# Performance work log

Hardware: AMD Instinct MI355X
Metric: run time of the kernel (lower is better)

The kernel has to match this reference:

```python
import jax, jax.numpy as jnp
import numpy as np

B, S, D = 2, 2048, 2048
H, KV, HD = 16, 8, 128
EPS = 1e-6
NEG = -1e9


def rms_norm(x, w, eps=EPS):
    # per-head RMSNorm over last dim, computed in fp32 like the torch module
    xf = x.astype(jnp.float32)
    var = jnp.mean(xf * xf, axis=-1, keepdims=True)
    return (w * (xf * jax.lax.rsqrt(var + eps)).astype(x.dtype))


def rotate_half(x):
    x1, x2 = jnp.split(x, 2, axis=-1)
    return jnp.concatenate((-x2, x1), axis=-1)


def setup_inputs() -> dict:
    key = jax.random.key(0)
    ks = jax.random.split(key, 8)
    hidden_states = jax.random.normal(ks[0], (B, S, D), dtype=jnp.float32)
    # RoPE tables (rope_theta=10000), shape [B, S, HD]
    inv_freq = 1.0 / (10000.0 ** (np.arange(0, HD, 2, dtype=np.float32) / HD))
    t = np.arange(S, dtype=np.float32)
    freqs = np.outer(t, inv_freq)                      # [S, HD/2]
    emb = np.concatenate([freqs, freqs], axis=-1)      # [S, HD]
    cos = jnp.broadcast_to(jnp.cos(emb)[None], (B, S, HD)).astype(jnp.float32)
    sin = jnp.broadcast_to(jnp.sin(emb)[None], (B, S, HD)).astype(jnp.float32)
    # additive causal mask [B, 1, S, S]
    causal = jnp.triu(jnp.full((S, S), NEG, dtype=jnp.float32), k=1)
    attention_mask = jnp.broadcast_to(causal[None, None], (B, 1, S, S))
    scale = 0.02
    Wq = jax.random.normal(ks[1], (D, H * HD), dtype=jnp.float32) * scale
    Wk = jax.random.normal(ks[2], (D, KV * HD), dtype=jnp.float32) * scale
    Wv = jax.random.normal(ks[3], (D, KV * HD), dtype=jnp.float32) * scale
    Wo = jax.random.normal(ks[4], (H * HD, D), dtype=jnp.float32) * scale
    q_norm_w = jnp.ones((HD,), dtype=jnp.float32)
    k_norm_w = jnp.ones((HD,), dtype=jnp.float32)
    return {"hidden_states": hidden_states, "cos": cos, "sin": sin,
            "attention_mask": attention_mask, "Wq": Wq, "Wk": Wk, "Wv": Wv,
            "Wo": Wo, "q_norm_w": q_norm_w, "k_norm_w": k_norm_w}


def reference(hidden_states, cos, sin, attention_mask, Wq, Wk, Wv, Wo, q_norm_w, k_norm_w):
    b, s, _ = hidden_states.shape
    scaling = HD ** -0.5
    n_rep = H // KV
    q = (hidden_states @ Wq).reshape(b, s, H, HD)
    k = (hidden_states @ Wk).reshape(b, s, KV, HD)
    v = (hidden_states @ Wv).reshape(b, s, KV, HD)
    # per-head RMSNorm then [B, heads, S, HD]
    q = rms_norm(q, q_norm_w).transpose(0, 2, 1, 3)
    k = rms_norm(k, k_norm_w).transpose(0, 2, 1, 3)
    v = v.transpose(0, 2, 1, 3)
    # RoPE (cos/sin unsqueezed on head axis)
    c = cos[:, None, :, :]
    sn = sin[:, None, :, :]
    q = q * c + rotate_half(q) * sn
    k = k * c + rotate_half(k) * sn
    # GQA: repeat kv heads
    k = jnp.repeat(k, n_rep, axis=1)
    v = jnp.repeat(v, n_rep, axis=1)
    scores = jnp.einsum('bhqd,bhkd->bhqk', q, k) * scaling + attention_mask
    probs = jax.nn.softmax(scores.astype(jnp.float32), axis=-1).astype(q.dtype)
    out = jnp.einsum('bhqk,bhkd->bhqd', probs, v)
    out = out.transpose(0, 2, 1, 3).reshape(b, s, H * HD)
    return out @ Wo
```

## Files before the change

### kernel.cpp

```cpp
#include <hip/hip_runtime.h>

typedef unsigned short u16;
typedef unsigned short u16x8 __attribute__((ext_vector_type(8)));
typedef short s16x8 __attribute__((ext_vector_type(8)));
typedef float f32x4 __attribute__((ext_vector_type(4)));
typedef float f32x16 __attribute__((ext_vector_type(16)));
typedef unsigned u32x4 __attribute__((ext_vector_type(4)));

__device__ __forceinline__ u16 f2b(float f){
  unsigned u = __builtin_bit_cast(unsigned, f);
  u += 0x7fffu + ((u >> 16) & 1u);
  return (u16)(u >> 16);
}
__device__ __forceinline__ float b2f(u16 v){
  unsigned u = ((unsigned)v) << 16;
  return __builtin_bit_cast(float, u);
}

#define MFMA16(c, a, b) (c) = __builtin_amdgcn_mfma_f32_16x16x32_bf16((a), (b), (c), 0, 0, 0)
#define MFMA32(c, a, b) (c) = __builtin_amdgcn_mfma_f32_32x32x16_bf16((a), (b), (c), 0, 0, 0)

__device__ __forceinline__ void gl16(const u16* g, char* l){
  __builtin_amdgcn_global_load_lds((const __attribute__((address_space(1))) void*)g,
                                   (__attribute__((address_space(3))) void*)l, 16, 0, 0);
}

__global__ void k_cast(const float* __restrict__ src, u16* __restrict__ dst, int n8){
  int i = blockIdx.x * blockDim.x + threadIdx.x;
  if (i >= n8) return;
  const float4* s = (const float4*)(src + (size_t)i * 8);
  float4 a = s[0], b = s[1];
  u16x8 o;
  o[0]=f2b(a.x); o[1]=f2b(a.y); o[2]=f2b(a.z); o[3]=f2b(a.w);
  o[4]=f2b(b.x); o[5]=f2b(b.y); o[6]=f2b(b.z); o[7]=f2b(b.w);
  *(u16x8*)(dst + (size_t)i * 8) = o;
}

__global__ void k_transpose(const float* __restrict__ src, u16* __restrict__ dst, int K, int N){
  __shared__ float t[32][33];
  int n0 = blockIdx.x * 32, k0 = blockIdx.y * 32;
  int c = threadIdx.x & 31, r4 = threadIdx.x >> 5;
  #pragma unroll
  for (int p = 0; p < 4; ++p){
    int r = r4 + p * 8;
    t[r][c] = src[(size_t)(k0 + r) * N + n0 + c];
  }
  __syncthreads();
  #pragma unroll
  for (int p = 0; p < 4; ++p){
    int r = r4 + p * 8;
    dst[(size_t)(n0 + r) * K + k0 + c] = f2b(t[c][r]);
  }
}

template<int NREP, bool OBF>
__global__ __launch_bounds__(512, 1) void k_gemm8(const u16* __restrict__ A, const u16* __restrict__ BT,
                                                  void* __restrict__ Cv, int M, int N, int K){
  constexpr int NH = NREP / 2;
  constexpr int BROWS = NREP * 32;
  constexpr int BLOADS = NREP / 2;
  constexpr int TOT = 4 + 2 * BLOADS;
  __shared__ __align__(16) u16 sA[2][2][128 * 64];
  __shared__ __align__(16) u16 sB[2][2][BROWS * 64];
  const int tid = threadIdx.x;
  const int lane = tid & 63, w = tid >> 6;
  const int l15 = lane & 15, l4 = lane >> 4;
  const int sx = l15 & 7;
  const int wr = w >> 2, wc = w & 3;
  const int m0 = blockIdx.y * 256, n0 = blockIdx.x * (NREP * 64);
  const int nk = K >> 6;

  f32x4 acc[8][NREP];
  #pragma unroll
  for (int mi = 0; mi < 8; ++mi)
    #pragma unroll
    for (int ni = 0; ni < NREP; ++ni) acc[mi][ni] = (f32x4){0.f, 0.f, 0.f, 0.f};

  auto stageA = [&](int d, int half, int k0){
    #pragma unroll
    for (int j = 0; j < 2; ++j){
      const int q = j * 512 + tid;
      const int r = q >> 3, cc = q & 7;
      gl16(A + (size_t)(m0 + half * 128 + r) * K + k0 + ((cc ^ (r & 7)) << 3),
           (char*)&sA[d][half][0] + j * 8192 + (tid >> 6) * 1024);
    }
  };
  auto stageB = [&](int d, int half, int k0){
    #pragma unroll
    for (int j = 0; j < BLOADS; ++j){
      const int q = j * 512 + tid;
      const int r = q >> 3, cc = q & 7;
      gl16(BT + (size_t)(n0 + half * BROWS + r) * K + k0 + ((cc ^ (r & 7)) << 3),
           (char*)&sB[d][half][0] + j * 8192 + (tid >> 6) * 1024);
    }
  };

  stageA(0, 0, 0); stageA(0, 1, 0); stageB(0, 0, 0); stageB(0, 1, 0);
  stageA(1, 0, 64); stageA(1, 1, 64); stageB(1, 0, 64); stageB(1, 1, 64);
  if constexpr (TOT == 8) asm volatile("s_waitcnt vmcnt(8)" ::: "memory");
  else                    asm volatile("s_waitcnt vmcnt(6)" ::: "memory");
  __builtin_amdgcn_s_barrier();

  const int halfB = wc >> 1;
  const int rb0 = (wc & 1) * (NREP * 16);

  for (int kt = 0; kt < nk; ++kt){
    const int d = kt & 1;
    const bool pre = (kt + 2) < nk;
    const int k0n = (kt + 2) << 6;
    const char* hA = (const char*)&sA[d][wr][0];
    const char* hB = (const char*)&sB[d][halfB][0];
    s16x8 aa[4][2], bb0[NH][2], bb1[NH][2];

    #pragma unroll
    for (int mi = 0; mi < 4; ++mi)
      #pragma unroll
      for (int kk = 0; kk < 2; ++kk)
        aa[mi][kk] = *(const s16x8*)(hA + (mi * 16 + l15) * 128 + (((kk * 4 + l4) ^ sx) << 4));
    #pragma unroll
    for (int ni = 0; ni < NH; ++ni)
      #pragma unroll
      for (int kk = 0; kk < 2; ++kk)
        bb0[ni][kk] = *(const s16x8*)(hB + (rb0 + ni * 16 + l15) * 128 + (((kk * 4 + l4) ^ sx) << 4));
    __builtin_amdgcn_s_setprio(1);
    #pragma unroll
    for (int mi = 0; mi < 4; ++mi)
      #pragma unroll
      for (int ni = 0; ni < NH; ++ni)
        #pragma unroll
        for (int kk = 0; kk < 2; ++kk)
          MFMA16(acc[mi][ni], aa[mi][kk], bb0[ni][kk]);
    __builtin_amdgcn_s_setprio(0);

    #pragma unroll
    for (int ni = 0; ni < NH; ++ni)
      #pragma unroll
      for (int kk = 0; kk < 2; ++kk)
        bb1[ni][kk] = *(const s16x8*)(hB + (rb0 + (NH + ni) * 16 + l15) * 128 + (((kk * 4 + l4) ^ sx) << 4));
    __builtin_amdgcn_s_setprio(1);
    #pragma unroll
    for (int mi = 0; mi < 4; ++mi)
      #pragma unroll
      for (int ni = 0; ni < NH; ++ni)
        #pragma unroll
        for (int kk = 0; kk < 2; ++kk)
          MFMA16(acc[mi][NH + ni], aa[mi][kk], bb1[ni][kk]);
    __builtin_amdgcn_s_setprio(0);
    __builtin_amdgcn_s_barrier();

    #pragma unroll
    for (int mi = 0; mi < 4; ++mi)
      #pragma unroll
      for (int kk = 0; kk < 2; ++kk)
        aa[mi][kk] = *(const s16x8*)(hA + ((mi + 4) * 16 + l15) * 128 + (((kk * 4 + l4) ^ sx) << 4));
    if (pre){ stageB(d, 0, k0n); stageB(d, 1, k0n); }
    __builtin_amdgcn_s_setprio(1);
    #pragma unroll
    for (int mi = 0; mi < 4; ++mi)
      #pragma unroll
      for (int ni = 0; ni < NH; ++ni)
        #pragma unroll
        for (int kk = 0; kk < 2; ++kk)
          MFMA16(acc[mi + 4][ni], aa[mi][kk], bb0[ni][kk]);
    __builtin_amdgcn_s_setprio(0);
    __builtin_amdgcn_s_barrier();

    if (pre){ stageA(d, 0, k0n); stageA(d, 1, k0n); }
    __builtin_amdgcn_s_setprio(1);
    #pragma unroll
    for (int mi = 0; mi < 4; ++mi)
      #pragma unroll
      for (int ni = 0; ni < NH; ++ni)
        #pragma unroll
        for (int kk = 0; kk < 2; ++kk)
          MFMA16(acc[mi + 4][NH + ni], aa[mi][kk], bb1[ni][kk]);
    __builtin_amdgcn_s_setprio(0);
    if (kt + 1 < nk){
      if (pre){
        if constexpr (TOT == 8) asm volatile("s_waitcnt vmcnt(8)" ::: "memory");
        else                    asm volatile("s_waitcnt vmcnt(6)" ::: "memory");
      } else {
        asm volatile("s_waitcnt vmcnt(0)" ::: "memory");
      }
      __builtin_amdgcn_s_barrier();
    }
  }

  #pragma unroll
  for (int mi = 0; mi < 8; ++mi)
    #pragma unroll
    for (int ni = 0; ni < NREP; ++ni)
      #pragma unroll
      for (int i = 0; i < 4; ++i){
        const int row = m0 + wr * 128 + mi * 16 + l4 * 4 + i;
        const int col = n0 + wc * (NREP * 16) + ni * 16 + l15;
        if constexpr (OBF) ((u16*)Cv)[(size_t)row * N + col] = f2b(acc[mi][ni][i]);
        else               ((float*)Cv)[(size_t)row * N + col] = acc[mi][ni][i];
      }
}

__global__ __launch_bounds__(256, 4) void k_rmsrope(const u16* __restrict__ qkvb,
    const float* __restrict__ cosT, const float* __restrict__ sinT,
    const float* __restrict__ qw, const float* __restrict__ kw,
    u16* __restrict__ qout, u16* __restrict__ kout, u16* __restrict__ vout){
  const int bs = blockIdx.x;
  const int b = bs >> 11, s = bs & 2047;
  const int lane = threadIdx.x & 63, w = threadIdx.x >> 6;
  const u16* row = qkvb + (size_t)bs * 4096;
  const float c1 = cosT[(size_t)bs * 128 + lane];
  const float s1 = sinT[(size_t)bs * 128 + lane];
  const float c2 = cosT[(size_t)bs * 128 + 64 + lane];
  const float s2 = sinT[(size_t)bs * 128 + 64 + lane];
  const float wq1 = qw[lane], wq2 = qw[64 + lane];
  const float wk1 = kw[lane], wk2 = kw[64 + lane];
  for (int u = w; u < 32; u += 4){
    if (u < 24){
      const int isq = (u < 16);
      const int base = isq ? u * 128 : 2048 + (u - 16) * 128;
      float x1 = b2f(row[base + lane]), x2 = b2f(row[base + 64 + lane]);
      float ss = x1 * x1 + x2 * x2;
      #pragma unroll
      for (int m = 1; m < 64; m <<= 1) ss += __shfl_xor(ss, m);
      float rsq = rsqrtf(ss * (1.0f / 128.0f) + 1e-6f);
      float n1 = x1 * rsq * (isq ? wq1 : wk1);
      float n2 = x2 * rsq * (isq ? wq2 : wk2);
      float o1 = n1 * c1 - n2 * s1;
      float o2 = n2 * c2 + n1 * s2;
      if (isq){
        size_t o = ((size_t)(b * 16 + u) * 2048 + s) * 128;
        qout[o + lane] = f2b(o1); qout[o + 64 + lane] = f2b(o2);
      } else {
        size_t o = ((size_t)(b * 8 + (u - 16)) * 2048 + s) * 128;
        kout[o + lane] = f2b(o1); kout[o + 64 + lane] = f2b(o2);
      }
    } else {
      const int j = u - 24;
      size_t o = ((size_t)(b * 8 + j) * 2048 + s) * 128;
      vout[o + lane] = row[3072 + j * 128 + lane];
      vout[o + 64 + lane] = row[3072 + j * 128 + 64 + lane];
    }
  }
}

__global__ __launch_bounds__(256, 8) void k_vtrans(const u16* __restrict__ v, u16* __restrict__ vt){
  __shared__ u16 t[64][130];
  const int bid = blockIdx.x;
  const int hd = bid >> 5, sb = bid & 31;
  const u16* src = v + (size_t)hd * 262144 + (size_t)sb * 64 * 128;
  u16* dst = vt + (size_t)hd * 262144 + sb * 64;
  const int tid = threadIdx.x;
  const int r = tid >> 2, c0 = (tid & 3) * 32;
  #pragma unroll
  for (int j = 0; j < 4; ++j)
    *(u16x8*)&t[r][c0 + j * 8] = *(const u16x8*)(src + r * 128 + c0 + j * 8);
  __syncthreads();
  const int d = tid >> 1, s0 = (tid & 1) * 32;
  #pragma unroll
  for (int j = 0; j < 4; ++j){
    u16x8 ov;
    #pragma unroll
    for (int e = 0; e < 8; ++e) ov[e] = t[s0 + j * 8 + e][d];
    *(u16x8*)(dst + (size_t)d * 2048 + s0 + j * 8) = ov;
  }
}

__device__ __forceinline__ void stage_kv(const u16* __restrict__ Kg, const u16* __restrict__ Vt,
                                         int kt, u16* sKb, u16* sVb, int tid){
  #pragma unroll
  for (int i = 0; i < 4; ++i){
    const int off = i * 4096 + tid * 16;
    const unsigned wub = (unsigned)(i * 4096 + (tid >> 6) * 1024);
    const int key = off >> 8, ks = (off >> 4) & 15;
    __builtin_amdgcn_global_load_lds(
        (const __attribute__((address_space(1))) void*)(Kg + (size_t)(kt * 64 + key) * 128 + ((ks ^ (key & 15)) << 3)),
        (__attribute__((address_space(3))) void*)((char*)sKb + wub), 16, 0, 0);
    const int d = off >> 7, vs = (off >> 4) & 7;
    __builtin_amdgcn_global_load_lds(
        (const __attribute__((address_space(1))) void*)(Vt + (size_t)d * 2048 + kt * 64 + ((vs ^ (d & 7)) << 3)),
        (__attribute__((address_space(3))) void*)((char*)sVb + wub), 16, 0, 0);
  }
}

__global__ __launch_bounds__(256, 2) void k_attn(const u16* __restrict__ qb, const u16* __restrict__ kb,
                                                 const u16* __restrict__ vtb, u16* __restrict__ ob){
  __shared__ __align__(128) u16 sK[2][64 * 128];
  __shared__ __align__(128) u16 sV[2][128 * 64];
  const int tid = threadIdx.x, lane = tid & 63, w = tid >> 6;
  const int hi = lane >> 5, l31 = lane & 31;
  const int bid = blockIdx.x;
  const int bh = bid & 31;
  const int kvh = bh & 7, r2 = bh >> 3;
  const int b = r2 >> 1, h = kvh * 2 + (r2 & 1);
  const int slot = bid >> 5;
  const int qt = (slot < 8) ? (15 - 2 * slot) : (2 * slot - 16);
  const u16* Q  = qb  + ((size_t)(b * 16 + h)  * 2048) * 128;
  const u16* Kg = kb  + ((size_t)(b * 8 + kvh) * 2048) * 128;
  const u16* Vt = vtb + ((size_t)(b * 8 + kvh) * 128) * 2048;
  const int qrow0 = qt * 128 + w * 32;

  s16x8 qf[8];
  #pragma unroll
  for (int ds = 0; ds < 8; ++ds)
    qf[ds] = *(const s16x8*)(Q + (size_t)(qrow0 + l31) * 128 + ds * 16 + hi * 8);

  f32x16 acc[4] = {};
  float mx = -1e30f, lsum = 0.f;
  const int nkt = qt * 2 + 2;

  stage_kv(Kg, Vt, 0, sK[0], sV[0], tid);
  for (int kt = 0; kt < nkt; ++kt){
    const int cur = kt & 1;
    if (kt + 1 < nkt){
      stage_kv(Kg, Vt, kt + 1, sK[cur ^ 1], sV[cur ^ 1], tid);
      asm volatile("s_waitcnt vmcnt(8)");
    } else {
      asm volatile("s_waitcnt vmcnt(0)");
    }
    __builtin_amdgcn_s_barrier();

    if (kt * 64 <= qrow0 + 31){
      const char* sKc = (const char*)sK[cur];
      const char* sVc = (const char*)sV[cur];
      f32x16 s0 = {}, s1 = {};
      #pragma unroll
      for (int ds = 0; ds < 8; ++ds){
        const int sl = ((ds * 2 + hi) ^ (l31 & 15)) << 4;
        s16x8 k0 = *(const s16x8*)(sKc + l31 * 256 + sl);
        s16x8 k1 = *(const s16x8*)(sKc + 8192 + l31 * 256 + sl);
        MFMA32(s0, k0, qf[ds]);
        MFMA32(s1, k1, qf[ds]);
      }
      const int qg = qrow0 + l31;
      const bool domask = (kt * 64 + 63) > qrow0;
      float pv0[16], pv1[16];
      float pmax = -1e30f;
      #pragma unroll
      for (int r = 0; r < 16; ++r){
        const int krow = (r & 3) + 8 * (r >> 2) + 4 * hi;
        float v0 = s0[r] * 0.08838834764831845f;
        float v1 = s1[r] * 0.08838834764831845f;
        if (domask){
          if (kt * 64 + krow > qg)      v0 = -1e30f;
          if (kt * 64 + 32 + krow > qg) v1 = -1e30f;
        }
        pv0[r] = v0; pv1[r] = v1;
        pmax = fmaxf(pmax, fmaxf(v0, v1));
      }
      pmax = fmaxf(pmax, __shfl_xor(pmax, 32));
      if (!__all(pmax - mx <= 8.f)){
        const float mn = fmaxf(mx, pmax);
        const float al = __expf(mx - mn);
        mx = mn; lsum *= al;
        #pragma unroll
        for (int r = 0; r < 16; ++r){
          const float ar = __shfl(al, (r & 3) + 8 * (r >> 2) + 4 * hi);
          acc[0][r] *= ar; acc[1][r] *= ar; acc[2][r] *= ar; acc[3][r] *= ar;
        }
      }
      float rs = 0.f;
      #pragma unroll
      for (int r = 0; r < 16; ++r){
        const float e0 = __expf(pv0[r] - mx);
        const float e1 = __expf(pv1[r] - mx);
        pv0[r] = e0; pv1[r] = e1;
        rs += e0 + e1;
      }
      rs += __shfl_xor(rs, 32);
      lsum += rs;
      #pragma unroll
      for (int s = 0; s < 4; ++s){
        const int t8 = (s & 1) * 8;
        unsigned w0, w1, w2, w3;
        if (s < 2){
          asm("v_cvt_pk_bf16_f32 %0, %1, %2" : "=v"(w0) : "v"(pv0[t8+0]), "v"(pv0[t8+1]));
          asm("v_cvt_pk_bf16_f32 %0, %1, %2" : "=v"(w1) : "v"(pv0[t8+2]), "v"(pv0[t8+3]));
          asm("v_cvt_pk_bf16_f32 %0, %1, %2" : "=v"(w2) : "v"(pv0[t8+4]), "v"(pv0[t8+5]));
          asm("v_cvt_pk_bf16_f32 %0, %1, %2" : "=v"(w3) : "v"(pv0[t8+6]), "v"(pv0[t8+7]));
        } else {
          asm("v_cvt_pk_bf16_f32 %0, %1, %2" : "=v"(w0) : "v"(pv1[t8+0]), "v"(pv1[t8+1]));
          asm("v_cvt_pk_bf16_f32 %0, %1, %2" : "=v"(w1) : "v"(pv1[t8+2]), "v"(pv1[t8+3]));
          asm("v_cvt_pk_bf16_f32 %0, %1, %2" : "=v"(w2) : "v"(pv1[t8+4]), "v"(pv1[t8+5]));
          asm("v_cvt_pk_bf16_f32 %0, %1, %2" : "=v"(w3) : "v"(pv1[t8+6]), "v"(pv1[t8+7]));
        }
        asm("v_permlane32_swap_b32 %0, %1" : "+v"(w0), "+v"(w2));
        asm("v_permlane32_swap_b32 %0, %1" : "+v"(w1), "+v"(w3));
        u32x4 pw = {w0, w1, w2, w3};
        s16x8 pa = __builtin_bit_cast(s16x8, pw);
        #pragma unroll
        for (int db = 0; db < 4; ++db){
          const int d = db * 32 + l31;
          s16x8 vf = *(const s16x8*)(sVc + d * 128 + (((s * 2 + hi) ^ (d & 7)) << 4));
          MFMA32(acc[db], pa, vf);
        }
      }
    }
    asm volatile("s_waitcnt lgkmcnt(0)");
    __builtin_amdgcn_s_barrier();
  }
  float li[16];
  #pragma unroll
  for (int r = 0; r < 16; ++r)
    li[r] = __shfl(lsum, (r & 3) + 8 * (r >> 2) + 4 * hi);
  #pragma unroll
  for (int db = 0; db < 4; ++db)
    #pragma unroll
    for (int r = 0; r < 16; ++r){
      const int row = qrow0 + (r & 3) + 8 * (r >> 2) + 4 * hi;
      const int col = h * 128 + db * 32 + l31;
      ob[((size_t)(b * 2048) + row) * 2048 + col] = f2b(acc[db][r] / li[r]);
    }
}

extern "C" void kernel_launch(void* const* d_in, const int* in_sizes, int n_in,
                              void* d_out, int out_size, void* d_ws, size_t ws_size,
                              hipStream_t stream){
  const float* hs   = (const float*)d_in[0];
  const float* cosT = (const float*)d_in[1];
  const float* sinT = (const float*)d_in[2];
  const float* Wq = (const float*)d_in[4];
  const float* Wk = (const float*)d_in[5];
  const float* Wv = (const float*)d_in[6];
  const float* Wo = (const float*)d_in[7];
  const float* qw = (const float*)d_in[8];
  const float* kw = (const float*)d_in[9];
  float* out = (float*)d_out;
  char* ws = (char*)d_ws;

  u16*   hsb   = (u16*)(ws);
  u16*   wqkvT = (u16*)(ws + 16777216);
  u16*   woT   = (u16*)(ws + 33554432);
  u16*   qkvb  = (u16*)(ws + 41943040);
  u16*   qb    = hsb;
  u16*   kb2   = (u16*)(ws + 16777216);
  u16*   vb2   = (u16*)(ws + 16777216 + 8388608);
  u16*   attnb = (u16*)(ws + 41943040);
  u16*   vtb   = (u16*)(ws + 41943040 + 16777216);

  k_cast<<<4096, 256, 0, stream>>>(hs, hsb, 1048576);
  k_transpose<<<dim3(64, 64),  256, 0, stream>>>(Wq, wqkvT,                       2048, 2048);
  k_transpose<<<dim3(32, 64),  256, 0, stream>>>(Wk, wqkvT + (size_t)2048 * 2048, 2048, 1024);
  k_transpose<<<dim3(32, 64),  256, 0, stream>>>(Wv, wqkvT + (size_t)3072 * 2048, 2048, 1024);
  k_transpose<<<dim3(64, 64),  256, 0, stream>>>(Wo, woT,                         2048, 2048);
  k_gemm8<4, true><<<dim3(16, 16), 512, 0, stream>>>(hsb, wqkvT, qkvb, 4096, 4096, 2048);
  k_rmsrope<<<4096, 256, 0, stream>>>(qkvb, cosT, sinT, qw, kw, qb, kb2, vb2);
  k_vtrans<<<512, 256, 0, stream>>>(vb2, vtb);
  k_attn<<<512, 256, 0, stream>>>(qb, kb2, vtb, attnb);
  k_gemm8<2, false><<<dim3(16, 16), 512, 0, stream>>>(attnb, woT, out, 4096, 2048, 2048);
}
```

Before: 228.2 us.

## Fuse RMSNorm and RoPE into QKV GEMM epilogue and merge weight transposes

Moves the per-head RMSNorm, RoPE and head-major scatter of Q/K/V into the QKV GEMM epilogue. Each 128-wide head is split across two waves, which exchange partial sums of squares and rotate-half partner values through shared memory. This removes the bf16 qkv intermediate round-trip and a separate kernel launch. The four weight-transpose launches are also merged into one grid. In exchange the epilogue gains extra barriers, register pressure, and stores that are scattered and only 2 bytes wide.

After: 209.6 us. 8.2% less time.

```diff
diff --git a/kernel.cpp b/kernel.cpp
--- a/kernel.cpp
+++ b/kernel.cpp
@@ -2,6 +2,7 @@
 
 typedef unsigned short u16;
 typedef unsigned short u16x8 __attribute__((ext_vector_type(8)));
+typedef unsigned short u16x4 __attribute__((ext_vector_type(4)));
 typedef short s16x8 __attribute__((ext_vector_type(8)));
 typedef float f32x4 __attribute__((ext_vector_type(4)));
 typedef float f32x16 __attribute__((ext_vector_type(16)));
@@ -36,9 +37,18 @@
   *(u16x8*)(dst + (size_t)i * 8) = o;
 }
 
-__global__ void k_transpose(const float* __restrict__ src, u16* __restrict__ dst, int K, int N){
+__global__ void k_transall(const float* __restrict__ Wq, const float* __restrict__ Wk,
+                           const float* __restrict__ Wv, const float* __restrict__ Wo,
+                           u16* __restrict__ wqkvT, u16* __restrict__ woT){
   __shared__ float t[32][33];
-  int n0 = blockIdx.x * 32, k0 = blockIdx.y * 32;
+  int by = blockIdx.y;
+  const float* src; u16* dst; int N;
+  if (by < 64)       { src = Wq; dst = wqkvT;                        N = 2048; }
+  else if (by < 128) { src = Wk; dst = wqkvT + (size_t)2048 * 2048;  N = 1024; by -= 64; }
+  else if (by < 192) { src = Wv; dst = wqkvT + (size_t)3072 * 2048;  N = 1024; by -= 128; }
+  else               { src = Wo; dst = woT;                          N = 2048; by -= 192; }
+  int n0 = blockIdx.x * 32, k0 = by * 32;
+  if (n0 >= N) return;
   int c = threadIdx.x & 31, r4 = threadIdx.x >> 5;
   #pragma unroll
   for (int p = 0; p < 4; ++p){
@@ -49,19 +59,25 @@
   #pragma unroll
   for (int p = 0; p < 4; ++p){
     int r = r4 + p * 8;
-    dst[(size_t)(n0 + r) * K + k0 + c] = f2b(t[c][r]);
-  }
-}
-
-template<int NREP, bool OBF>
+    dst[(size_t)(n0 + r) * 2048 + k0 + c] = f2b(t[c][r]);
+  }
+}
+
+template<int NREP, int MODE>
 __global__ __launch_bounds__(512, 1) void k_gemm8(const u16* __restrict__ A, const u16* __restrict__ BT,
-                                                  void* __restrict__ Cv, int M, int N, int K){
+                                                  float* __restrict__ Cv, int M, int N, int K,
+                                                  u16* __restrict__ qout, u16* __restrict__ kout,
+                                                  u16* __restrict__ vout,
+                                                  const float* __restrict__ cosT, const float* __restrict__ sinT,
+                                                  const float* __restrict__ qw, const float* __restrict__ kw){
   constexpr int NH = NREP / 2;
   constexpr int BROWS = NREP * 32;
   constexpr int BLOADS = NREP / 2;
   constexpr int TOT = 4 + 2 * BLOADS;
-  __shared__ __align__(16) u16 sA[2][2][128 * 64];
-  __shared__ __align__(16) u16 sB[2][2][BROWS * 64];
+  constexpr int SMEM = 65536 + 2 * 2 * BROWS * 64 * 2;
+  __shared__ __align__(128) char smem[SMEM];
+  u16* sAp = (u16*)smem;
+  u16* sBp = (u16*)(smem + 65536);
   const int tid = threadIdx.x;
   const int lane = tid & 63, w = tid >> 6;
   const int l15 = lane & 15, l4 = lane >> 4;
@@ -82,7 +98,7 @@
       const int q = j * 512 + tid;
       const int r = q >> 3, cc = q & 7;
       gl16(A + (size_t)(m0 + half * 128 + r) * K + k0 + ((cc ^ (r & 7)) << 3),
-           (char*)&sA[d][half][0] + j * 8192 + (tid >> 6) * 1024);
+           (char*)(sAp + (d * 2 + half) * 8192) + j * 8192 + (tid >> 6) * 1024);
     }
   };
   auto stageB = [&](int d, int half, int k0){
@@ -91,7 +107,7 @@
       const int q = j * 512 + tid;
       const int r = q >> 3, cc = q & 7;
       gl16(BT + (size_t)(n0 + half * BROWS + r) * K + k0 + ((cc ^ (r & 7)) << 3),
-           (char*)&sB[d][half][0] + j * 8192 + (tid >> 6) * 1024);
+           (char*)(sBp + (d * 2 + half) * (BROWS * 64)) + j * 8192 + (tid >> 6) * 1024);
     }
   };
 
@@ -108,8 +124,8 @@
     const int d = kt & 1;
     const bool pre = (kt + 2) < nk;
     const int k0n = (kt + 2) << 6;
-    const char* hA = (const char*)&sA[d][wr][0];
-    const char* hB = (const char*)&sB[d][halfB][0];
+    const char* hA = (const char*)(sAp + (d * 2 + wr) * 8192);
+    const char* hB = (const char*)(sBp + (d * 2 + halfB) * (BROWS * 64));
     s16x8 aa[4][2], bb0[NH][2], bb1[NH][2];
 
     #pragma unroll
@@ -186,58 +202,114 @@
     }
   }
 
-  #pragma unroll
-  for (int mi = 0; mi < 8; ++mi)
-    #pragma unroll
-    for (int ni = 0; ni < NREP; ++ni)
-      #pragma unroll
-      for (int i = 0; i < 4; ++i){
-        const int row = m0 + wr * 128 + mi * 16 + l4 * 4 + i;
-        const int col = n0 + wc * (NREP * 16) + ni * 16 + l15;
-        if constexpr (OBF) ((u16*)Cv)[(size_t)row * N + col] = f2b(acc[mi][ni][i]);
-        else               ((float*)Cv)[(size_t)row * N + col] = acc[mi][ni][i];
-      }
-}
-
-__global__ __launch_bounds__(256, 4) void k_rmsrope(const u16* __restrict__ qkvb,
-    const float* __restrict__ cosT, const float* __restrict__ sinT,
-    const float* __restrict__ qw, const float* __restrict__ kw,
-    u16* __restrict__ qout, u16* __restrict__ kout, u16* __restrict__ vout){
-  const int bs = blockIdx.x;
-  const int b = bs >> 11, s = bs & 2047;
-  const int lane = threadIdx.x & 63, w = threadIdx.x >> 6;
-  const u16* row = qkvb + (size_t)bs * 4096;
-  const float c1 = cosT[(size_t)bs * 128 + lane];
-  const float s1 = sinT[(size_t)bs * 128 + lane];
-  const float c2 = cosT[(size_t)bs * 128 + 64 + lane];
-  const float s2 = sinT[(size_t)bs * 128 + 64 + lane];
-  const float wq1 = qw[lane], wq2 = qw[64 + lane];
-  const float wk1 = kw[lane], wk2 = kw[64 + lane];
-  for (int u = w; u < 32; u += 4){
+  if constexpr (MODE == 0){
+    #pragma unroll
+    for (int mi = 0; mi < 8; ++mi)
+      #pragma unroll
+      for (int ni = 0; ni < NREP; ++ni)
+        #pragma unroll
+        for (int i = 0; i < 4; ++i){
+          const int row = m0 + wr * 128 + mi * 16 + l4 * 4 + i;
+          const int col = n0 + wc * (NREP * 16) + ni * 16 + l15;
+          Cv[(size_t)row * N + col] = acc[mi][ni][i];
+        }
+  } else {
+    const int u    = (n0 >> 7) + (wc >> 1);
+    const int half = wc & 1;
+    __syncthreads();
+    float ss[32];
     if (u < 24){
-      const int isq = (u < 16);
-      const int base = isq ? u * 128 : 2048 + (u - 16) * 128;
-      float x1 = b2f(row[base + lane]), x2 = b2f(row[base + 64 + lane]);
-      float ss = x1 * x1 + x2 * x2;
-      #pragma unroll
-      for (int m = 1; m < 64; m <<= 1) ss += __shfl_xor(ss, m);
-      float rsq = rsqrtf(ss * (1.0f / 128.0f) + 1e-6f);
-      float n1 = x1 * rsq * (isq ? wq1 : wk1);
-      float n2 = x2 * rsq * (isq ? wq2 : wk2);
-      float o1 = n1 * c1 - n2 * s1;
-      float o2 = n2 * c2 + n1 * s2;
-      if (isq){
-        size_t o = ((size_t)(b * 16 + u) * 2048 + s) * 128;
-        qout[o + lane] = f2b(o1); qout[o + 64 + lane] = f2b(o2);
-      } else {
-        size_t o = ((size_t)(b * 8 + (u - 16)) * 2048 + s) * 128;
-        kout[o + lane] = f2b(o1); kout[o + 64 + lane] = f2b(o2);
+      #pragma unroll
+      for (int mi = 0; mi < 8; ++mi)
+        #pragma unroll
+        for (int i = 0; i < 4; ++i){
+          float s2 = 0.f;
+          #pragma unroll
+          for (int ni = 0; ni < 4; ++ni){ float x = acc[mi][ni][i]; s2 += x * x; }
+          ss[mi * 4 + i] = s2;
+        }
+      #pragma unroll
+      for (int off = 1; off < 16; off <<= 1)
+        #pragma unroll
+        for (int r = 0; r < 32; ++r) ss[r] += __shfl_xor(ss[r], off);
+      float* sums = (float*)smem;
+      if (l15 == 0){
+        #pragma unroll
+        for (int mi = 0; mi < 8; ++mi)
+          #pragma unroll
+          for (int i = 0; i < 4; ++i)
+            sums[(wr * 4 + wc) * 128 + mi * 16 + l4 * 4 + i] = ss[mi * 4 + i];
       }
     } else {
-      const int j = u - 24;
-      size_t o = ((size_t)(b * 8 + j) * 2048 + s) * 128;
-      vout[o + lane] = row[3072 + j * 128 + lane];
-      vout[o + 64 + lane] = row[3072 + j * 128 + 64 + lane];
+      #pragma unroll
+      for (int mi = 0; mi < 8; ++mi)
+        #pragma unroll
+        for (int ni = 0; ni < 4; ++ni)
+          #pragma unroll
+          for (int i = 0; i < 4; ++i){
+            const int rowi = m0 + wr * 128 + mi * 16 + l4 * 4 + i;
+            const int b_ = rowi >> 11, s_ = rowi & 2047;
+            const int d = half * 64 + ni * 16 + l15;
+            vout[((size_t)(b_ * 8 + (u - 24)) * 2048 + s_) * 128 + d] = f2b(acc[mi][ni][i]);
+          }
+    }
+    __syncthreads();
+    if (u < 24){
+      const float* sums = (const float*)smem;
+      #pragma unroll
+      for (int mi = 0; mi < 8; ++mi)
+        #pragma unroll
+        for (int i = 0; i < 4; ++i){
+          float tot = ss[mi * 4 + i] + sums[(wr * 4 + (wc ^ 1)) * 128 + mi * 16 + l4 * 4 + i];
+          ss[mi * 4 + i] = rsqrtf(tot * (1.0f / 128.0f) + 1e-6f);
+        }
+      const float* wvp = (u < 16) ? qw : kw;
+      float wn[4];
+      #pragma unroll
+      for (int ni = 0; ni < 4; ++ni) wn[ni] = wvp[half * 64 + ni * 16 + l15];
+      #pragma unroll
+      for (int mi = 0; mi < 8; ++mi)
+        #pragma unroll
+        for (int ni = 0; ni < 4; ++ni)
+          #pragma unroll
+          for (int i = 0; i < 4; ++i)
+            acc[mi][ni][i] *= ss[mi * 4 + i] * wn[ni];
+    }
+    __syncthreads();
+    u16* scr = (u16*)smem;
+    if (u < 24){
+      #pragma unroll
+      for (int mi = 0; mi < 8; ++mi)
+        #pragma unroll
+        for (int ni = 0; ni < 4; ++ni){
+          u16x4 pk;
+          #pragma unroll
+          for (int i = 0; i < 4; ++i) pk[i] = f2b(acc[mi][ni][i]);
+          *(u16x4*)(scr + ((((wr * 4 + wc) * 8 + mi) * 4 + ni) * 256) + (l4 * 16 + l15) * 4) = pk;
+        }
+    }
+    __syncthreads();
+    if (u < 24){
+      #pragma unroll
+      for (int mi = 0; mi < 8; ++mi){
+        #pragma unroll
+        for (int ni = 0; ni < 4; ++ni){
+          u16x4 pk = *(const u16x4*)(scr + ((((wr * 4 + (wc ^ 1)) * 8 + mi) * 4 + ni) * 256) + (l4 * 16 + l15) * 4);
+          const int d = half * 64 + ni * 16 + l15;
+          #pragma unroll
+          for (int i = 0; i < 4; ++i){
+            const int rowi = m0 + wr * 128 + mi * 16 + l4 * 4 + i;
+            const int b_ = rowi >> 11, s_ = rowi & 2047;
+            const float cs = cosT[(size_t)rowi * 128 + d];
+            const float sn = sinT[(size_t)rowi * 128 + d];
+            const float self = acc[mi][ni][i];
+            const float part = b2f(pk[i]);
+            const float o = half ? (self * cs + part * sn) : (self * cs - part * sn);
+            if (u < 16) qout[((size_t)(b_ * 16 + u) * 2048 + s_) * 128 + d] = f2b(o);
+            else        kout[((size_t)(b_ * 8 + (u - 16)) * 2048 + s_) * 128 + d] = f2b(o);
+          }
+        }
+      }
     }
   }
 }
@@ -426,24 +498,21 @@
   float* out = (float*)d_out;
   char* ws = (char*)d_ws;
 
-  u16*   hsb   = (u16*)(ws);
-  u16*   wqkvT = (u16*)(ws + 16777216);
-  u16*   woT   = (u16*)(ws + 33554432);
-  u16*   qkvb  = (u16*)(ws + 41943040);
-  u16*   qb    = hsb;
-  u16*   kb2   = (u16*)(ws + 16777216);
-  u16*   vb2   = (u16*)(ws + 16777216 + 8388608);
-  u16*   attnb = (u16*)(ws + 41943040);
-  u16*   vtb   = (u16*)(ws + 41943040 + 16777216);
+  u16* hsb   = (u16*)(ws);
+  u16* wqkvT = (u16*)(ws + ((size_t)16 << 20));
+  u16* woT   = (u16*)(ws + ((size_t)32 << 20));
+  u16* qb    = (u16*)(ws + ((size_t)40 << 20));
+  u16* kb2   = (u16*)(ws + ((size_t)56 << 20));
+  u16* vb2   = (u16*)(ws + ((size_t)64 << 20));
+  u16* vtb   = (u16*)(ws + ((size_t)72 << 20));
+  u16* attnb = (u16*)(ws + ((size_t)80 << 20));
 
   k_cast<<<4096, 256, 0, stream>>>(hs, hsb, 1048576);
-  k_transpose<<<dim3(64, 64),  256, 0, stream>>>(Wq, wqkvT,                       2048, 2048);
-  k_transpose<<<dim3(32, 64),  256, 0, stream>>>(Wk, wqkvT + (size_t)2048 * 2048, 2048, 1024);
-  k_transpose<<<dim3(32, 64),  256, 0, stream>>>(Wv, wqkvT + (size_t)3072 * 2048, 2048, 1024);
-  k_transpose<<<dim3(64, 64),  256, 0, stream>>>(Wo, woT,                         2048, 2048);
-  k_gemm8<4, true><<<dim3(16, 16), 512, 0, stream>>>(hsb, wqkvT, qkvb, 4096, 4096, 2048);
-  k_rmsrope<<<4096, 256, 0, stream>>>(qkvb, cosT, sinT, qw, kw, qb, kb2, vb2);
+  k_transall<<<dim3(64, 256), 256, 0, stream>>>(Wq, Wk, Wv, Wo, wqkvT, woT);
+  k_gemm8<4, 1><<<dim3(16, 16), 512, 0, stream>>>(hsb, wqkvT, nullptr, 4096, 4096, 2048,
+                                                  qb, kb2, vb2, cosT, sinT, qw, kw);
   k_vtrans<<<512, 256, 0, stream>>>(vb2, vtb);
   k_attn<<<512, 256, 0, stream>>>(qb, kb2, vtb, attnb);
-  k_gemm8<2, false><<<dim3(16, 16), 512, 0, stream>>>(attnb, woT, out, 4096, 2048, 2048);
-}
+  k_gemm8<2, 0><<<dim3(16, 16), 512, 0, stream>>>(attnb, woT, (float*)out, 4096, 2048, 2048,
+                                                  nullptr, nullptr, nullptr, nullptr, nullptr, nullptr, nullptr);
+}
```
